# Optimization experiments

Hardware: AMD Instinct MI355X
Metric: run time of the kernel (lower is better)

Reference implementation:

```python
import jax, jax.numpy as jnp
import numpy as np

B, T, H = 4, 4096, 2048
G_EPS = 0.5
LN_EPS = 1e-5
INIT_STD = 0.02


def setup_inputs() -> dict:
    key = jax.random.key(0)
    ks = jax.random.split(key, 4)
    return {
        "hidden_states": jax.random.normal(ks[0], (B, T, H), jnp.float32),
        "W_z": jax.random.normal(ks[1], (H, H), jnp.float32) * INIT_STD,
        "b_z": jnp.zeros((H,), jnp.float32),
        "W_h": jax.random.normal(ks[2], (H, H), jnp.float32) * INIT_STD,
        "b_h": jnp.zeros((H,), jnp.float32),
        "ln_w": jnp.ones((H,), jnp.float32),
        "ln_b": jnp.zeros((H,), jnp.float32),
        "h0": jax.random.normal(ks[3], (H,), jnp.float32) * INIT_STD,
    }


def _g_log(x):
    # torch.where(x >= 0, log(relu(x) + g_eps), -softplus(-x))
    return jnp.where(x >= 0, jnp.log(jax.nn.relu(x) + G_EPS), -jax.nn.softplus(-x))


def reference(hidden_states, W_z, b_z, W_h, b_h, ln_w, ln_b, h0):
    Bc, Tc, Hc = hidden_states.shape
    k = hidden_states @ W_z.T + b_z                      # [B,T,H]
    log_z = -jax.nn.softplus(-k)                         # log sigmoid(k)
    log_coeffs = -jax.nn.softplus(k)                     # log(1 - sigmoid(k))
    log_tilde_h = _g_log(hidden_states @ W_h.T + b_h)    # [B,T,H]
    log_h0 = jnp.broadcast_to(_g_log(h0), (Bc, 1, Hc))
    log_values = jnp.concatenate([log_h0, log_z + log_tilde_h], axis=1)  # [B,T+1,H]
    # NOTE: faithful to source: cumsum over the LAST (hidden) dim, then pad one
    # zero row at the front of the time dim (F.pad(..., (0,0,1,0))).
    a_star = jnp.pad(jnp.cumsum(log_coeffs, axis=-1), ((0, 0), (1, 0), (0, 0)))  # [B,T+1,H]
    log_h = a_star + jax.lax.cumlogsumexp(log_values - a_star, axis=1)
    # global mean / unbiased std normalization, as in source
    log_h = (log_h - log_h.mean()) / jnp.std(log_h, ddof=1)
    h = jnp.exp(log_h)[:, 1:, :]                         # drop the h0 step
    # residual + LayerNorm (dropout is identity in eval)
    x = h + hidden_states
    mu = x.mean(axis=-1, keepdims=True)
    var = x.var(axis=-1, keepdims=True)
    return (x - mu) * jax.lax.rsqrt(var + LN_EPS) * ln_w + ln_b
```

## Files before the change

### kernel.cpp

```cpp
#include <hip/hip_runtime.h>
#include <stdint.h>

constexpr int NB = 4;
constexpr int NT = 4096;
constexpr int NH = 2048;
constexpr int MROWS = NB * NT;
constexpr int TP1 = NT + 1;
constexpr int CH2 = 17;
constexpr int NCH2 = 241;
constexpr int GSZ = 16;
constexpr int NGRP = (NCH2 + GSZ - 1) / GSZ;
constexpr int NCOL = NB * NH;

typedef unsigned short u16;
typedef __bf16 bf16x8 __attribute__((ext_vector_type(8)));
typedef float f32x4 __attribute__((ext_vector_type(4)));
typedef unsigned short u16x8 __attribute__((ext_vector_type(8)));
typedef _Float16 h16x8 __attribute__((ext_vector_type(8)));
typedef u16x8 __attribute__((may_alias)) u16x8_a;
typedef h16x8 __attribute__((may_alias)) h16x8_a;
typedef float4 __attribute__((may_alias)) float4_a;

__device__ __forceinline__ u16 f2bf(float f) {
  unsigned int u = __float_as_uint(f);
  return (u16)((u + 0x7fffu + ((u >> 16) & 1u)) >> 16);
}
__device__ __forceinline__ float bf2f(u16 v) {
  return __uint_as_float(((unsigned int)v) << 16);
}
__device__ __forceinline__ float spf_(float x) {
  return fmaxf(x, 0.f) + __logf(1.f + __expf(-fabsf(x)));
}
__device__ __forceinline__ float glogf_(float x) {
  return (x >= 0.f) ? __logf(x + 0.5f) : -spf_(-x);
}
__device__ __forceinline__ void gld16(const void* g, void* l) {
  __builtin_amdgcn_global_load_lds((const __attribute__((address_space(1))) void*)g,
                                   (__attribute__((address_space(3))) void*)l, 16, 0, 0);
}
__device__ __forceinline__ void ld8(const float* p, float* r) {
  float4 a = *(const float4_a*)p, b = *(const float4_a*)(p + 4);
  r[0] = a.x; r[1] = a.y; r[2] = a.z; r[3] = a.w;
  r[4] = b.x; r[5] = b.y; r[6] = b.z; r[7] = b.w;
}
__device__ __forceinline__ void st8(float* p, const float* r) {
  *(float4_a*)p       = make_float4(r[0], r[1], r[2], r[3]);
  *(float4_a*)(p + 4) = make_float4(r[4], r[5], r[6], r[7]);
}
__device__ __forceinline__ void lsecomb(float& M, float& S, float Mo, float So) {
  const float Mn = fmaxf(M, Mo);
  float Sn = S * __expf(M - Mn) + So * __expf(Mo - Mn);
  if (Mn == -INFINITY) Sn = 0.f;
  M = Mn; S = Sn;
}

__global__ __launch_bounds__(256) void cvt_all(
    const float* __restrict__ hs, const float* __restrict__ Wz,
    const float* __restrict__ Wh, u16* __restrict__ hsb,
    u16* __restrict__ wzb, u16* __restrict__ whb) {
  const int s0 = MROWS * NH / 8;
  const int s1 = s0 + NH * NH / 8;
  const int s2 = s1 + NH * NH / 8;
  int i = blockIdx.x * 256 + threadIdx.x;
  if (i >= s2) return;
  const float* in; u16* out; int j;
  if (i < s0)      { in = hs; out = hsb; j = i; }
  else if (i < s1) { in = Wz; out = wzb; j = i - s0; }
  else             { in = Wh; out = whb; j = i - s1; }
  const float4* p = (const float4*)in;
  float4 a = p[2 * (size_t)j], b = p[2 * (size_t)j + 1];
  u16x8 o;
  o[0] = f2bf(a.x); o[1] = f2bf(a.y); o[2] = f2bf(a.z); o[3] = f2bf(a.w);
  o[4] = f2bf(b.x); o[5] = f2bf(b.y); o[6] = f2bf(b.z); o[7] = f2bf(b.w);
  *(u16x8*)(out + (size_t)j * 8) = o;
}

__global__ __launch_bounds__(256, 4) void gemm_bt(
    const u16* __restrict__ A,
    const u16* __restrict__ Bz, const u16* __restrict__ Bh,
    const float* __restrict__ bz, const float* __restrict__ bh,
    u16* __restrict__ KU) {
  const u16* Bm  = blockIdx.y ? Bh : Bz;
  const float* bias = blockIdx.y ? bh : bz;
  u16* Cw = KU + (blockIdx.y ? 2048 : 0);

  const int bid = blockIdx.x;
  const int wg = (bid & 7) * 256 + (bid >> 3);
  const int bx = wg & 15;
  const int by = wg >> 4;
  const int row0 = by << 7, col0 = bx << 7;

  __shared__ u16 ldsA[128 * 64];
  __shared__ u16 ldsB[128 * 64];

  const int tid = threadIdx.x;
  const int lane = tid & 63;
  const int wv = tid >> 6;
  const int wr = (wv >> 1) << 6;
  const int wc = (wv & 1) << 6;

  const int srow = lane >> 3;
  const int sslot = ((lane & 7) ^ srow) << 3;
  const int xsw = (lane & 7) << 3;
  const int q8 = (lane >> 4) << 3;
  const int f15 = lane & 15;

  f32x4 acc[4][4] = {};

  for (int k0 = 0; k0 < NH; k0 += 64) {
    if (k0) __syncthreads();
#pragma unroll
    for (int i = 0; i < 4; ++i) {
      const int r = i * 32 + wv * 8 + srow;
      const size_t gcol = (size_t)(k0 + sslot);
      gld16(A  + (size_t)(row0 + r) * NH + gcol, &ldsA[(size_t)(i * 256 + wv * 64) * 8]);
      gld16(Bm + (size_t)(col0 + r) * NH + gcol, &ldsB[(size_t)(i * 256 + wv * 64) * 8]);
    }
    __syncthreads();
#pragma unroll
    for (int ks = 0; ks < 2; ++ks) {
      const int cphys = ((ks << 5) | q8) ^ xsw;
      bf16x8 af[4], bfr[4];
#pragma unroll
      for (int m = 0; m < 4; ++m)
        af[m] = *(const bf16x8*)&ldsA[(wr + m * 16 + f15) * 64 + cphys];
#pragma unroll
      for (int n = 0; n < 4; ++n)
        bfr[n] = *(const bf16x8*)&ldsB[(wc + n * 16 + f15) * 64 + cphys];
#pragma unroll
      for (int m = 0; m < 4; ++m)
#pragma unroll
        for (int n = 0; n < 4; ++n)
          acc[m][n] = __builtin_amdgcn_mfma_f32_16x16x32_bf16(af[m], bfr[n], acc[m][n], 0, 0, 0);
    }
  }

  const int fr = lane & 15, fq = lane >> 4;
#pragma unroll
  for (int n = 0; n < 4; ++n) {
    const int col = col0 + wc + n * 16 + fr;
    const float bv = bias[col];
#pragma unroll
    for (int m = 0; m < 4; ++m) {
#pragma unroll
      for (int v = 0; v < 4; ++v) {
        const int row = row0 + wr + m * 16 + fq * 4 + v;
        Cw[(size_t)row * 4096 + col] = f2bf(acc[m][n][v] + bv);
      }
    }
  }
}

__device__ __forceinline__ void row_pointwise(const char* KU, size_t row,
                                              int tid, float* lc, float* lv) {
  const size_t rb = row * 8192;
  u16x8 kv = *(const u16x8_a*)(KU + rb + tid * 16);
  u16x8 uv = *(const u16x8_a*)(KU + rb + 4096 + tid * 16);
#pragma unroll
  for (int e = 0; e < 8; ++e) {
    const float k = bf2f(kv[e]);
    const float L = __logf(1.f + __expf(-fabsf(k)));
    lc[e] = -fmaxf(k, 0.f) - L;
    lv[e] = fminf(k, 0.f) - L + glogf_(bf2f(uv[e]));
  }
}

__global__ __launch_bounds__(256) void carry_pass(
    const char* __restrict__ KU, float* __restrict__ cm, float* __restrict__ cs,
    const float* __restrict__ h0) {
  const int ch = blockIdx.x;
  const int b = blockIdx.y;
  const int tid = threadIdx.x;
  const int lane = tid & 63, wvx = tid >> 6;
  const int t0 = ch * CH2;
  const int t1 = (t0 + CH2 < TP1) ? (t0 + CH2) : TP1;

  float m8[8], s8[8];
#pragma unroll
  for (int e = 0; e < 8; ++e) { m8[e] = -INFINITY; s8[e] = 0.f; }

  __shared__ float wsum[2][4];

  float lc[8], lv[8];
  {
    const int tf = (t0 < 1) ? 1 : t0;
    if (tf < t1) row_pointwise(KU, (size_t)b * NT + (tf - 1), tid, lc, lv);
  }

  for (int tt = t0; tt < t1; ++tt) {
    if (tt == 0) {
#pragma unroll
      for (int e = 0; e < 8; ++e) {
        const float x = glogf_(h0[tid * 8 + e]);
        m8[e] = x; s8[e] = 1.f;
      }
      continue;
    }
    float nlc[8], nlv[8];
    const bool pf = (tt + 1 < t1);
    if (pf) row_pointwise(KU, (size_t)b * NT + tt, tid, nlc, nlv);

    float cum[8], run = 0.f;
#pragma unroll
    for (int e = 0; e < 8; ++e) { run += lc[e]; cum[e] = run; }
    float v = run;
#pragma unroll
    for (int d = 1; d < 64; d <<= 1) {
      float o = __shfl_up(v, d, 64);
      if (lane >= d) v += o;
    }
    const int par = tt & 1;
    if (lane == 63) wsum[par][wvx] = v;
    __syncthreads();
    float base = v - run;
#pragma unroll
    for (int w = 0; w < 4; ++w)
      if (w < wvx) base += wsum[par][w];

#pragma unroll
    for (int e = 0; e < 8; ++e) {
      const float x = lv[e] - (base + cum[e]);
      const float nm = fmaxf(m8[e], x);
      s8[e] = s8[e] * __expf(m8[e] - nm) + __expf(x - nm);
      m8[e] = nm;
    }
    if (pf) {
#pragma unroll
      for (int e = 0; e < 8; ++e) { lc[e] = nlc[e]; lv[e] = nlv[e]; }
    }
  }
  const size_t co = ((size_t)ch * NB + b) * NH + tid * 8;
  st8(cm + co, m8);
  st8(cs + co, s8);
}

__global__ __launch_bounds__(256) void carry_groupred(
    const float* __restrict__ cm, const float* __restrict__ cs,
    float* __restrict__ gm, float* __restrict__ gs) {
  const int c = blockIdx.x * 256 + threadIdx.x;
  const int g = blockIdx.y;
  const int ch0 = g * GSZ;
  const int ch1 = (ch0 + GSZ < NCH2) ? (ch0 + GSZ) : NCH2;
  float M = -INFINITY, S = 0.f;
  for (int ch = ch0; ch < ch1; ++ch) {
    const size_t o = (size_t)ch * NCOL + c;
    lsecomb(M, S, cm[o], cs[o]);
  }
  gm[(size_t)g * NCOL + c] = M;
  gs[(size_t)g * NCOL + c] = S;
}

__global__ __launch_bounds__(256) void carry_groupscan(float* __restrict__ gm,
                                                       float* __restrict__ gs) {
  const int c = blockIdx.x * 256 + threadIdx.x;
  float M = -INFINITY, S = 0.f;
  for (int g = 0; g < NGRP; ++g) {
    const size_t o = (size_t)g * NCOL + c;
    const float m2 = gm[o], s2 = gs[o];
    gm[o] = M; gs[o] = S;
    lsecomb(M, S, m2, s2);
  }
}

__global__ __launch_bounds__(256) void carry_apply(
    float* __restrict__ cm, float* __restrict__ cs,
    const float* __restrict__ gm, const float* __restrict__ gs) {
  const int c = blockIdx.x * 256 + threadIdx.x;
  const int g = blockIdx.y;
  const int ch0 = g * GSZ;
  const int ch1 = (ch0 + GSZ < NCH2) ? (ch0 + GSZ) : NCH2;
  float M = gm[(size_t)g * NCOL + c];
  float S = gs[(size_t)g * NCOL + c];
  for (int ch = ch0; ch < ch1; ++ch) {
    const size_t o = (size_t)ch * NCOL + c;
    const float m2 = cm[o], s2 = cs[o];
    cm[o] = M; cs[o] = S;
    lsecomb(M, S, m2, s2);
  }
}

__global__ __launch_bounds__(256) void scan_final(
    const char* __restrict__ KU, _Float16* __restrict__ LH16,
    const float* __restrict__ cm, const float* __restrict__ cs,
    const float* __restrict__ h0, double* __restrict__ sums) {
  const int ch = blockIdx.x;
  const int b = blockIdx.y;
  const int tid = threadIdx.x;
  const int lane = tid & 63, wvx = tid >> 6;
  const int t0 = ch * CH2;
  const int t1 = (t0 + CH2 < TP1) ? (t0 + CH2) : TP1;

  float m8[8], s8[8];
  {
    const size_t co = ((size_t)ch * NB + b) * NH + tid * 8;
    ld8(cm + co, m8);
    ld8(cs + co, s8);
  }

  __shared__ float wsum[2][4];
  double s1 = 0.0, s2 = 0.0;

  float lc[8], lv[8];
  {
    const int tf = (t0 < 1) ? 1 : t0;
    if (tf < t1) row_pointwise(KU, (size_t)b * NT + (tf - 1), tid, lc, lv);
  }

  for (int tt = t0; tt < t1; ++tt) {
    if (tt == 0) {
#pragma unroll
      for (int e = 0; e < 8; ++e) {
        const float x = glogf_(h0[tid * 8 + e]);
        m8[e] = x; s8[e] = 1.f;
        s1 += (double)x;
        s2 += (double)x * (double)x;
      }
      continue;
    }
    float nlc[8], nlv[8];
    const bool pf = (tt + 1 < t1);
    if (pf) row_pointwise(KU, (size_t)b * NT + tt, tid, nlc, nlv);

    float cum[8], run = 0.f;
#pragma unroll
    for (int e = 0; e < 8; ++e) { run += lc[e]; cum[e] = run; }
    float v = run;
#pragma unroll
    for (int d = 1; d < 64; d <<= 1) {
      float o = __shfl_up(v, d, 64);
      if (lane >= d) v += o;
    }
    const int par = tt & 1;
    if (lane == 63) wsum[par][wvx] = v;
    __syncthreads();
    float base = v - run;
#pragma unroll
    for (int w = 0; w < 4; ++w)
      if (w < wvx) base += wsum[par][w];

    h16x8 lhv;
#pragma unroll
    for (int e = 0; e < 8; ++e) {
      const float as = base + cum[e];
      const float x = lv[e] - as;
      const float nm = fmaxf(m8[e], x);
      s8[e] = s8[e] * __expf(m8[e] - nm) + __expf(x - nm);
      m8[e] = nm;
      const float lh = as + nm + __logf(s8[e]);
      lhv[e] = (_Float16)lh;
      s1 += (double)lh;
      s2 += (double)lh * (double)lh;
    }
    const size_t row = (size_t)b * NT + (tt - 1);
    *(h16x8_a*)(LH16 + row * NH + tid * 8) = lhv;
    if (pf) {
#pragma unroll
      for (int e = 0; e < 8; ++e) { lc[e] = nlc[e]; lv[e] = nlv[e]; }
    }
  }
  double v1 = s1, v2 = s2;
#pragma unroll
  for (int d = 32; d; d >>= 1) {
    v1 += __shfl_down(v1, d, 64);
    v2 += __shfl_down(v2, d, 64);
  }
  __shared__ double dr1[4], dr2[4];
  if (lane == 0) { dr1[wvx] = v1; dr2[wvx] = v2; }
  __syncthreads();
  if (tid == 0) {
    atomicAdd(&sums[0], dr1[0] + dr1[1] + dr1[2] + dr1[3]);
    atomicAdd(&sums[1], dr2[0] + dr2[1] + dr2[2] + dr2[3]);
  }
}

__global__ void finalize_stats(const double* __restrict__ sums,
                               float* __restrict__ stats) {
  const double S = sums[0], S2 = sums[1];
  const double N = (double)NB * (double)TP1 * (double)NH;
  const double mu = S / N;
  const double var = (S2 - S * S / N) / (N - 1.0);
  stats[0] = (float)mu;
  stats[1] = (float)(1.0 / sqrt(var));
}

__global__ __launch_bounds__(256) void final_ln(
    float* __restrict__ OUT, const _Float16* __restrict__ LH16,
    const u16* __restrict__ hsb,
    const float* __restrict__ lnw, const float* __restrict__ lnb,
    const float* __restrict__ stats) {
  const int tid = threadIdx.x;
  const size_t off = (size_t)blockIdx.x * NH + tid * 8;
  const float mu_g = stats[0], isd = stats[1];

  float lh[8], av[8];
  {
    h16x8 hv = *(const h16x8_a*)(LH16 + off);
#pragma unroll
    for (int e = 0; e < 8; ++e) lh[e] = (float)hv[e];
  }
  {
    u16x8 hv = *(const u16x8_a*)(hsb + off);
#pragma unroll
    for (int e = 0; e < 8; ++e) av[e] = bf2f(hv[e]);
  }
  float x[8];
  float s = 0.f, q = 0.f;
#pragma unroll
  for (int e = 0; e < 8; ++e) {
    x[e] = __expf((lh[e] - mu_g) * isd) + av[e];
    s += x[e];
    q += x[e] * x[e];
  }
#pragma unroll
  for (int d = 32; d; d >>= 1) {
    s += __shfl_down(s, d, 64);
    q += __shfl_down(q, d, 64);
  }
  __shared__ float r1[4], r2[4];
  const int lane = tid & 63, wvx = tid >> 6;
  if (lane == 0) { r1[wvx] = s; r2[wvx] = q; }
  __syncthreads();
  const float st = r1[0] + r1[1] + r1[2] + r1[3];
  const float qt = r2[0] + r2[1] + r2[2] + r2[3];
  const float mean = st * (1.0f / NH);
  const float var = qt * (1.0f / NH) - mean * mean;
  const float rstd = rsqrtf(var + 1e-5f);

  float wv8[8], bv8[8];
  ld8(lnw + tid * 8, wv8);
  ld8(lnb + tid * 8, bv8);
  float o[8];
#pragma unroll
  for (int e = 0; e < 8; ++e)
    o[e] = (x[e] - mean) * rstd * wv8[e] + bv8[e];
  st8(OUT + off, o);
}

extern "C" void kernel_launch(void* const* d_in, const int* in_sizes, int n_in,
                              void* d_out, int out_size, void* d_ws, size_t ws_size,
                              hipStream_t stream) {
  (void)in_sizes; (void)n_in; (void)out_size; (void)ws_size;
  const float* hs  = (const float*)d_in[0];
  const float* Wz  = (const float*)d_in[1];
  const float* bz  = (const float*)d_in[2];
  const float* Wh  = (const float*)d_in[3];
  const float* bh  = (const float*)d_in[4];
  const float* lnw = (const float*)d_in[5];
  const float* lnb = (const float*)d_in[6];
  const float* h0  = (const float*)d_in[7];
  float* out = (float*)d_out;

  char* w = (char*)d_ws;
  u16* hsb   = (u16*)w;  w += (size_t)MROWS * NH * 2;
  u16* wzb   = (u16*)w;  w += (size_t)NH * NH * 2;
  u16* whb   = (u16*)w;  w += (size_t)NH * NH * 2;
  char* KU   = w;        w += (size_t)MROWS * 8192;
  double* sums = (double*)w; w += 16;
  float* stats = (float*)w;  w += 64;
  float* gm_ = (float*)w;    w += (size_t)NGRP * NCOL * 4;
  float* gs_ = (float*)w;    w += (size_t)NGRP * NCOL * 4;
  _Float16* LH16 = (_Float16*)w; w += (size_t)MROWS * NH * 2;
  float* cm_ = (float*)wzb;
  float* cs_ = cm_ + (size_t)NCH2 * NCOL;

  hipMemsetAsync(sums, 0, 16, stream);

  {
    const int tot8 = MROWS * NH / 8 + 2 * (NH * NH / 8);
    cvt_all<<<dim3((tot8 + 255) / 256), 256, 0, stream>>>(hs, Wz, Wh, hsb, wzb, whb);
  }

  gemm_bt<<<dim3((MROWS / 128) * (NH / 128), 2), 256, 0, stream>>>(
      hsb, wzb, whb, bz, bh, (u16*)KU);

  carry_pass<<<dim3(NCH2, NB), 256, 0, stream>>>(KU, cm_, cs_, h0);

  carry_groupred<<<dim3(NCOL / 256, NGRP), 256, 0, stream>>>(cm_, cs_, gm_, gs_);
  carry_groupscan<<<dim3(NCOL / 256), 256, 0, stream>>>(gm_, gs_);
  carry_apply<<<dim3(NCOL / 256, NGRP), 256, 0, stream>>>(cm_, cs_, gm_, gs_);

  scan_final<<<dim3(NCH2, NB), 256, 0, stream>>>(KU, LH16, cm_, cs_, h0, sums);
  finalize_stats<<<1, 1, 0, stream>>>(sums, stats);

  final_ln<<<dim3(MROWS), 256, 0, stream>>>(out, LH16, hsb, lnw, lnb, stats);
}
```

Before: 541.5 us.

## Use 32x32 MFMA in GEMM, fold stats finalize into LN, nontemporal stores

Switches the bf16 GEMM from 16x16x32 to 32x32x16 MFMA tiles, with a 2x2 accumulator layout per wave and a new epilogue index mapping. This aims to cut LDS fragment reads per MFMA and raise matrix-core throughput. The single-thread finalize_stats kernel is removed and its computation folded into each final_ln block, saving one launch at the cost of redundant double math per block. The LayerNorm output now uses nontemporal stores to avoid polluting the cache.

After: 575.0 us. +6.2%, slower.

```diff
diff --git a/kernel.cpp b/kernel.cpp
--- a/kernel.cpp
+++ b/kernel.cpp
@@ -14,12 +14,14 @@
 
 typedef unsigned short u16;
 typedef __bf16 bf16x8 __attribute__((ext_vector_type(8)));
-typedef float f32x4 __attribute__((ext_vector_type(4)));
+typedef float f32x16 __attribute__((ext_vector_type(16)));
+typedef float f32x4v __attribute__((ext_vector_type(4)));
 typedef unsigned short u16x8 __attribute__((ext_vector_type(8)));
 typedef _Float16 h16x8 __attribute__((ext_vector_type(8)));
 typedef u16x8 __attribute__((may_alias)) u16x8_a;
 typedef h16x8 __attribute__((may_alias)) h16x8_a;
 typedef float4 __attribute__((may_alias)) float4_a;
+typedef f32x4v __attribute__((may_alias)) f32x4v_a;
 
 __device__ __forceinline__ u16 f2bf(float f) {
   unsigned int u = __float_as_uint(f);
@@ -46,6 +48,12 @@
 __device__ __forceinline__ void st8(float* p, const float* r) {
   *(float4_a*)p       = make_float4(r[0], r[1], r[2], r[3]);
   *(float4_a*)(p + 4) = make_float4(r[4], r[5], r[6], r[7]);
+}
+__device__ __forceinline__ void st8_nt(float* p, const float* r) {
+  f32x4v a = {r[0], r[1], r[2], r[3]};
+  f32x4v b = {r[4], r[5], r[6], r[7]};
+  __builtin_nontemporal_store(a, (f32x4v_a*)p);
+  __builtin_nontemporal_store(b, (f32x4v_a*)(p + 4));
 }
 __device__ __forceinline__ void lsecomb(float& M, float& S, float Mo, float So) {
   const float Mn = fmaxf(M, Mo);
@@ -75,7 +83,7 @@
   *(u16x8*)(out + (size_t)j * 8) = o;
 }
 
-__global__ __launch_bounds__(256, 4) void gemm_bt(
+__global__ __launch_bounds__(256, 4) void gemm_bt32(
     const u16* __restrict__ A,
     const u16* __restrict__ Bz, const u16* __restrict__ Bh,
     const float* __restrict__ bz, const float* __restrict__ bh,
@@ -96,16 +104,16 @@
   const int tid = threadIdx.x;
   const int lane = tid & 63;
   const int wv = tid >> 6;
-  const int wr = (wv >> 1) << 6;
-  const int wc = (wv & 1) << 6;
+  const int wrow = (wv >> 1) << 6;
+  const int wcol = (wv & 1) << 6;
 
   const int srow = lane >> 3;
   const int sslot = ((lane & 7) ^ srow) << 3;
   const int xsw = (lane & 7) << 3;
-  const int q8 = (lane >> 4) << 3;
-  const int f15 = lane & 15;
-
-  f32x4 acc[4][4] = {};
+  const int kq8 = (lane >> 5) << 3;
+  const int f31 = lane & 31;
+
+  f32x16 acc[2][2] = {};
 
   for (int k0 = 0; k0 < NH; k0 += 64) {
     if (k0) __syncthreads();
@@ -118,34 +126,34 @@
     }
     __syncthreads();
 #pragma unroll
-    for (int ks = 0; ks < 2; ++ks) {
-      const int cphys = ((ks << 5) | q8) ^ xsw;
-      bf16x8 af[4], bfr[4];
-#pragma unroll
-      for (int m = 0; m < 4; ++m)
-        af[m] = *(const bf16x8*)&ldsA[(wr + m * 16 + f15) * 64 + cphys];
-#pragma unroll
-      for (int n = 0; n < 4; ++n)
-        bfr[n] = *(const bf16x8*)&ldsB[(wc + n * 16 + f15) * 64 + cphys];
-#pragma unroll
-      for (int m = 0; m < 4; ++m)
-#pragma unroll
-        for (int n = 0; n < 4; ++n)
-          acc[m][n] = __builtin_amdgcn_mfma_f32_16x16x32_bf16(af[m], bfr[n], acc[m][n], 0, 0, 0);
-    }
-  }
-
-  const int fr = lane & 15, fq = lane >> 4;
-#pragma unroll
-  for (int n = 0; n < 4; ++n) {
-    const int col = col0 + wc + n * 16 + fr;
+    for (int ks = 0; ks < 4; ++ks) {
+      const int cphys = ((ks << 4) | kq8) ^ xsw;
+      bf16x8 af[2], bfr[2];
+#pragma unroll
+      for (int m = 0; m < 2; ++m)
+        af[m] = *(const bf16x8*)&ldsA[(wrow + m * 32 + f31) * 64 + cphys];
+#pragma unroll
+      for (int n = 0; n < 2; ++n)
+        bfr[n] = *(const bf16x8*)&ldsB[(wcol + n * 32 + f31) * 64 + cphys];
+#pragma unroll
+      for (int m = 0; m < 2; ++m)
+#pragma unroll
+        for (int n = 0; n < 2; ++n)
+          acc[m][n] = __builtin_amdgcn_mfma_f32_32x32x16_bf16(af[m], bfr[n], acc[m][n], 0, 0, 0);
+    }
+  }
+
+  const int rhi = (lane >> 5) << 2;
+#pragma unroll
+  for (int n = 0; n < 2; ++n) {
+    const int col = col0 + wcol + n * 32 + f31;
     const float bv = bias[col];
 #pragma unroll
-    for (int m = 0; m < 4; ++m) {
-#pragma unroll
-      for (int v = 0; v < 4; ++v) {
-        const int row = row0 + wr + m * 16 + fq * 4 + v;
-        Cw[(size_t)row * 4096 + col] = f2bf(acc[m][n][v] + bv);
+    for (int m = 0; m < 2; ++m) {
+#pragma unroll
+      for (int r = 0; r < 16; ++r) {
+        const int row = row0 + wrow + m * 32 + (r & 3) + ((r >> 2) << 3) + rhi;
+        Cw[(size_t)row * 4096 + col] = f2bf(acc[m][n][r] + bv);
       }
     }
   }
@@ -373,24 +381,25 @@
   }
 }
 
-__global__ void finalize_stats(const double* __restrict__ sums,
-                               float* __restrict__ stats) {
-  const double S = sums[0], S2 = sums[1];
-  const double N = (double)NB * (double)TP1 * (double)NH;
-  const double mu = S / N;
-  const double var = (S2 - S * S / N) / (N - 1.0);
-  stats[0] = (float)mu;
-  stats[1] = (float)(1.0 / sqrt(var));
-}
-
 __global__ __launch_bounds__(256) void final_ln(
     float* __restrict__ OUT, const _Float16* __restrict__ LH16,
     const u16* __restrict__ hsb,
     const float* __restrict__ lnw, const float* __restrict__ lnb,
-    const float* __restrict__ stats) {
+    const double* __restrict__ sums) {
   const int tid = threadIdx.x;
   const size_t off = (size_t)blockIdx.x * NH + tid * 8;
-  const float mu_g = stats[0], isd = stats[1];
+
+  __shared__ float sstat[2];
+  if (tid == 0) {
+    const double S = sums[0], S2 = sums[1];
+    const double N = (double)NB * (double)TP1 * (double)NH;
+    const double mu = S / N;
+    const double var = (S2 - S * S / N) / (N - 1.0);
+    sstat[0] = (float)mu;
+    sstat[1] = (float)(1.0 / sqrt(var));
+  }
+  __syncthreads();
+  const float mu_g = sstat[0], isd = sstat[1];
 
   float lh[8], av[8];
   {
@@ -433,7 +442,7 @@
 #pragma unroll
   for (int e = 0; e < 8; ++e)
     o[e] = (x[e] - mean) * rstd * wv8[e] + bv8[e];
-  st8(OUT + off, o);
+  st8_nt(OUT + off, o);
 }
 
 extern "C" void kernel_launch(void* const* d_in, const int* in_sizes, int n_in,
@@ -456,7 +465,7 @@
   u16* whb   = (u16*)w;  w += (size_t)NH * NH * 2;
   char* KU   = w;        w += (size_t)MROWS * 8192;
   double* sums = (double*)w; w += 16;
-  float* stats = (float*)w;  w += 64;
+  float* stats = (float*)w;  w += 64; (void)stats;
   float* gm_ = (float*)w;    w += (size_t)NGRP * NCOL * 4;
   float* gs_ = (float*)w;    w += (size_t)NGRP * NCOL * 4;
   _Float16* LH16 = (_Float16*)w; w += (size_t)MROWS * NH * 2;
@@ -470,7 +479,7 @@
     cvt_all<<<dim3((tot8 + 255) / 256), 256, 0, stream>>>(hs, Wz, Wh, hsb, wzb, whb);
   }
 
-  gemm_bt<<<dim3((MROWS / 128) * (NH / 128), 2), 256, 0, stream>>>(
+  gemm_bt32<<<dim3((MROWS / 128) * (NH / 128), 2), 256, 0, stream>>>(
       hsb, wzb, whb, bz, bh, (u16*)KU);
 
   carry_pass<<<dim3(NCH2, NB), 256, 0, stream>>>(KU, cm_, cs_, h0);
@@ -480,7 +489,6 @@
   carry_apply<<<dim3(NCOL / 256, NGRP), 256, 0, stream>>>(cm_, cs_, gm_, gs_);
 
   scan_final<<<dim3(NCH2, NB), 256, 0, stream>>>(KU, LH16, cm_, cs_, h0, sums);
-  finalize_stats<<<1, 1, 0, stream>>>(sums, stats);
-
-  final_ln<<<dim3(MROWS), 256, 0, stream>>>(out, LH16, hsb, lnw, lnb, stats);
-}
+
+  final_ln<<<dim3(MROWS), 256, 0, stream>>>(out, LH16, hsb, lnw, lnb, sums);
+}
```
